# Kernel optimization log

Hardware: AMD Instinct MI355X
Metric: run time of the kernel (lower is better)

## Reference

```python
import jax, jax.numpy as jnp
import numpy as np


def setup_inputs() -> dict:
    key = jax.random.key(0)
    ks = jax.random.split(key, 7)
    B, T, E, H = 256, 512, 256, 256
    s = 1.0 / np.sqrt(E + H)
    return {
        "embedding": jax.random.normal(ks[0], (B, T, E), dtype=jnp.float32),
        "Wz": jax.random.normal(ks[1], (H, E + H), dtype=jnp.float32) * s,
        "bz": jax.random.normal(ks[2], (H,), dtype=jnp.float32) * s,
        "Wr": jax.random.normal(ks[3], (H, E + H), dtype=jnp.float32) * s,
        "br": jax.random.normal(ks[4], (H,), dtype=jnp.float32) * s,
        "Wm": jax.random.normal(ks[5], (H, E + H), dtype=jnp.float32) * s,
        "bm": jax.random.normal(ks[6], (H,), dtype=jnp.float32) * s,
    }


def reference(embedding, Wz, bz, Wr, br, Wm, bm):
    # embedding: [B, T, E] -> time-major [T, B, E] (matches Encoder.forward transpose)
    emb = jnp.transpose(embedding, (1, 0, 2))
    B = emb.shape[1]
    H = Wz.shape[0]
    h0 = jnp.zeros((B, H), dtype=embedding.dtype)

    def step(h, x):  # x: [B, E], h: [B, H]
        xi = jnp.concatenate([x, h], axis=1)            # [B, E+H]
        z = jax.nn.sigmoid(xi @ Wz.T + bz)              # update gate
        r = jax.nn.sigmoid(xi @ Wr.T + br)              # reset gate
        xm = jnp.concatenate([x, r * h], axis=1)
        h_cand = jnp.tanh(xm @ Wm.T + bm)
        h_new = (1.0 - z) * h + z * h_cand
        return h_new, h_new

    _, hs = jax.lax.scan(step, h0, emb)                 # hs: [T, B, H]
    return jnp.transpose(hs, (1, 0, 2))                 # [B, T, H]
```

## Files before the change

kernel.cpp:

```cpp
#include <hip/hip_runtime.h>

typedef _Float16 half8_t __attribute__((ext_vector_type(8)));
typedef _Float16 half2_t __attribute__((ext_vector_type(2)));
typedef float floatx4 __attribute__((ext_vector_type(4)));

#define B_DIM 256
#define T_DIM 512
#define E_DIM 256
#define H_DIM 256
#define MROWS (B_DIM * T_DIM)

__device__ __forceinline__ half2_t mk2(_Float16 x, _Float16 y) {
    half2_t v; v[0] = x; v[1] = y; return v;
}

__device__ __forceinline__ float fdot2f(half2_t a, half2_t b, float c) {
#if __has_builtin(__builtin_amdgcn_fdot2)
    return __builtin_amdgcn_fdot2(a, b, c, false);
#else
    return c + (float)a[0] * (float)b[0] + (float)a[1] * (float)b[1];
#endif
}

__global__ __launch_bounds__(256, 2) void gemm_x(
    const float* __restrict__ emb,
    const float* __restrict__ Wz, const float* __restrict__ bz,
    const float* __restrict__ Wr, const float* __restrict__ br,
    const float* __restrict__ Wm, const float* __restrict__ bm,
    _Float16* __restrict__ Xz, _Float16* __restrict__ Xr,
    float* __restrict__ Xm)
{
    const int n0 = blockIdx.x * 128;
    const int m0 = blockIdx.y * 128;
    const int gate = n0 >> 8;
    const int ng0 = n0 & 255;
    const float* W    = (gate == 0) ? Wz : (gate == 1) ? Wr : Wm;
    const float* bias = (gate == 0) ? bz : (gate == 1) ? br : bm;

    __shared__ __align__(16) _Float16 lA[128 * 40];
    __shared__ __align__(16) _Float16 lB[128 * 40];

    const int t = threadIdx.x;
    const int lane = t & 63;
    const int wave = t >> 6;
    const int wm = (wave >> 1) * 64;
    const int wn = (wave & 1) * 64;
    const int lq = lane >> 4;
    const int lr = lane & 15;

    floatx4 acc[4][4];
    #pragma unroll
    for (int i = 0; i < 4; ++i)
        #pragma unroll
        for (int j = 0; j < 4; ++j)
            acc[i][j] = (floatx4)0.0f;

    const int srow = t >> 1;
    const int scol = (t & 1) * 16;
    const float* aSrc = emb + (size_t)(m0 + srow) * E_DIM + scol;
    const float* bSrc = W + (size_t)(ng0 + srow) * (E_DIM + H_DIM) + scol;

    for (int k0 = 0; k0 < E_DIM; k0 += 32) {
        float ta[16], tb[16];
        #pragma unroll
        for (int u = 0; u < 4; ++u) {
            *(float4*)(ta + 4 * u) = *(const float4*)(aSrc + k0 + 4 * u);
            *(float4*)(tb + 4 * u) = *(const float4*)(bSrc + k0 + 4 * u);
        }
        half8_t a0, a1, b0, b1;
        #pragma unroll
        for (int u = 0; u < 8; ++u) {
            a0[u] = (_Float16)ta[u]; a1[u] = (_Float16)ta[u + 8];
            b0[u] = (_Float16)tb[u]; b1[u] = (_Float16)tb[u + 8];
        }
        __syncthreads();
        *(half8_t*)&lA[srow * 40 + scol]     = a0;
        *(half8_t*)&lA[srow * 40 + scol + 8] = a1;
        *(half8_t*)&lB[srow * 40 + scol]     = b0;
        *(half8_t*)&lB[srow * 40 + scol + 8] = b1;
        __syncthreads();

        half8_t af[4], bf[4];
        #pragma unroll
        for (int i = 0; i < 4; ++i)
            af[i] = *(const half8_t*)&lA[(wm + i * 16 + lr) * 40 + lq * 8];
        #pragma unroll
        for (int j = 0; j < 4; ++j)
            bf[j] = *(const half8_t*)&lB[(wn + j * 16 + lr) * 40 + lq * 8];
        #pragma unroll
        for (int i = 0; i < 4; ++i)
            #pragma unroll
            for (int j = 0; j < 4; ++j)
                acc[i][j] = __builtin_amdgcn_mfma_f32_16x16x32_f16(
                    af[i], bf[j], acc[i][j], 0, 0, 0);
    }

    if (gate < 2) {
        _Float16* dst = (gate == 0) ? Xz : Xr;
        #pragma unroll
        for (int j = 0; j < 4; ++j) {
            const int ng = ng0 + wn + j * 16 + lr;
            const float bv = bias[ng];
            #pragma unroll
            for (int i = 0; i < 4; ++i) {
                const int mrow = m0 + wm + i * 16 + lq * 4;
                #pragma unroll
                for (int r = 0; r < 4; ++r)
                    dst[(size_t)(mrow + r) * H_DIM + ng] =
                        (_Float16)(acc[i][j][r] + bv);
            }
        }
    } else {
        #pragma unroll
        for (int j = 0; j < 4; ++j) {
            const int ng = ng0 + wn + j * 16 + lr;
            const float bv = bias[ng];
            #pragma unroll
            for (int i = 0; i < 4; ++i) {
                const int mrow = m0 + wm + i * 16 + lq * 4;
                #pragma unroll
                for (int r = 0; r < 4; ++r)
                    Xm[(size_t)(mrow + r) * H_DIM + ng] = acc[i][j][r] + bv;
            }
        }
    }
}

__global__ __launch_bounds__(512, 2) void gru_rec(
    const float* __restrict__ Wz,
    const float* __restrict__ Wr,
    const float* __restrict__ Wm,
    const _Float16* __restrict__ Xz,
    const _Float16* __restrict__ Xr,
    float* __restrict__ out)
{
    const int b = blockIdx.x;
    const int t = threadIdx.x;
    const int jA = t & 255;
    const int jB = t >> 1;
    const int hB = t & 1;

    __shared__ __align__(16) _Float16 hh[256];
    __shared__ float hf[256];
    __shared__ __align__(16) _Float16 rh[256];
    __shared__ float zl[256];

    half2_t w1[128];
    {
        const float* wrow = ((t < 256) ? Wz : Wr) + (size_t)jA * 512 + 256;
        #pragma unroll
        for (int k = 0; k < 64; ++k) {
            float4 f = ((const float4*)wrow)[k];
            w1[2 * k]     = mk2((_Float16)f.x, (_Float16)f.y);
            w1[2 * k + 1] = mk2((_Float16)f.z, (_Float16)f.w);
        }
    }
    half2_t w2[64];
    {
        const float* wrow = Wm + (size_t)jB * 512 + 256 + hB * 128;
        #pragma unroll
        for (int k = 0; k < 32; ++k) {
            float4 f = ((const float4*)wrow)[k];
            w2[2 * k]     = mk2((_Float16)f.x, (_Float16)f.y);
            w2[2 * k + 1] = mk2((_Float16)f.z, (_Float16)f.w);
        }
    }

    if (t < 256) { hh[t] = (_Float16)0.0f; hf[t] = 0.0f; }
    __syncthreads();

    const size_t rowbase = (size_t)b * T_DIM * H_DIM;
    float xa_n = (t < 256) ? (float)Xz[rowbase + jA] : (float)Xr[rowbase + jA];
    float xm_n = (hB == 0) ? out[rowbase + jB] : 0.0f;

    for (int ts = 0; ts < T_DIM; ++ts) {
        const float xa = xa_n;
        const float xm = xm_n;
        if (ts + 1 < T_DIM) {
            const size_t nb = rowbase + (size_t)(ts + 1) * H_DIM;
            xa_n = (t < 256) ? (float)Xz[nb + jA] : (float)Xr[nb + jA];
            xm_n = (hB == 0) ? out[nb + jB] : 0.0f;
        }

        float a0 = xa, a1 = 0.f, a2 = 0.f, a3 = 0.f;
        const half8_t* hp8 = (const half8_t*)hh;
        #pragma unroll
        for (int k = 0; k < 32; ++k) {
            half8_t hv = hp8[k];
            a0 = fdot2f(w1[4 * k],     mk2(hv[0], hv[1]), a0);
            a1 = fdot2f(w1[4 * k + 1], mk2(hv[2], hv[3]), a1);
            a2 = fdot2f(w1[4 * k + 2], mk2(hv[4], hv[5]), a2);
            a3 = fdot2f(w1[4 * k + 3], mk2(hv[6], hv[7]), a3);
        }
        const float a = (a0 + a1) + (a2 + a3);
        const float g = 1.0f / (1.0f + __expf(-a));
        if (t < 256) zl[jA] = g;
        else         rh[jA] = (_Float16)(g * hf[jA]);
        __syncthreads();

        float c0 = 0.f, c1 = 0.f;
        const half8_t* rp8 = (const half8_t*)(rh + hB * 128);
        #pragma unroll
        for (int k = 0; k < 16; ++k) {
            half8_t rv = rp8[k];
            c0 = fdot2f(w2[4 * k],     mk2(rv[0], rv[1]), c0);
            c1 = fdot2f(w2[4 * k + 1], mk2(rv[2], rv[3]), c1);
            c0 = fdot2f(w2[4 * k + 2], mk2(rv[4], rv[5]), c0);
            c1 = fdot2f(w2[4 * k + 3], mk2(rv[6], rv[7]), c1);
        }
        float c = c0 + c1;
        c += __shfl_xor(c, 1);
        if (hB == 0) {
            const float am = c + xm;
            const float hcand = 2.0f / (1.0f + __expf(-2.0f * am)) - 1.0f;
            const float z = zl[jB];
            const float hn = (1.0f - z) * hf[jB] + z * hcand;
            out[rowbase + (size_t)ts * H_DIM + jB] = hn;
            hf[jB] = hn;
            hh[jB] = (_Float16)hn;
        }
        __syncthreads();
    }
}

extern "C" void kernel_launch(void* const* d_in, const int* in_sizes, int n_in,
                              void* d_out, int out_size, void* d_ws, size_t ws_size,
                              hipStream_t stream) {
    (void)in_sizes; (void)n_in; (void)out_size; (void)ws_size;
    const float* emb = (const float*)d_in[0];
    const float* Wz  = (const float*)d_in[1];
    const float* bz  = (const float*)d_in[2];
    const float* Wr  = (const float*)d_in[3];
    const float* br  = (const float*)d_in[4];
    const float* Wm  = (const float*)d_in[5];
    const float* bm  = (const float*)d_in[6];
    float* out = (float*)d_out;

    _Float16* Xz = (_Float16*)d_ws;
    _Float16* Xr = Xz + (size_t)MROWS * H_DIM;

    dim3 g1(6, MROWS / 128);
    gemm_x<<<g1, 256, 0, stream>>>(emb, Wz, bz, Wr, br, Wm, bm, Xz, Xr, out);
    gru_rec<<<B_DIM, 512, 0, stream>>>(Wz, Wr, Wm, Xz, Xr, out);
}
```

Baseline: 1.190 ms.

## Use MFMA for recurrent matvecs in GRU step instead of fdot2 loops

Result: faster. 1.019 ms (-14.3%).

```diff
diff --git a/kernel.cpp b/kernel.cpp
--- a/kernel.cpp
+++ b/kernel.cpp
@@ -12,14 +12,6 @@
 
 __device__ __forceinline__ half2_t mk2(_Float16 x, _Float16 y) {
     half2_t v; v[0] = x; v[1] = y; return v;
-}
-
-__device__ __forceinline__ float fdot2f(half2_t a, half2_t b, float c) {
-#if __has_builtin(__builtin_amdgcn_fdot2)
-    return __builtin_amdgcn_fdot2(a, b, c, false);
-#else
-    return c + (float)a[0] * (float)b[0] + (float)a[1] * (float)b[1];
-#endif
 }
 
 __global__ __launch_bounds__(256, 2) void gemm_x(
@@ -126,6 +118,12 @@
     }
 }
 
+__device__ __forceinline__ float pick4(floatx4 v, int r) {
+    float x01 = (r & 1) ? v[1] : v[0];
+    float x23 = (r & 1) ? v[3] : v[2];
+    return (r & 2) ? x23 : x01;
+}
+
 __global__ __launch_bounds__(512, 2) void gru_rec(
     const float* __restrict__ Wz,
     const float* __restrict__ Wr,
@@ -136,88 +134,121 @@
 {
     const int b = blockIdx.x;
     const int t = threadIdx.x;
-    const int jA = t & 255;
-    const int jB = t >> 1;
-    const int hB = t & 1;
+    const int w    = t >> 6;
+    const int lane = t & 63;
+    const int lr   = lane & 15;
+    const int lq   = lane >> 4;
 
     __shared__ __align__(16) _Float16 hh[256];
-    __shared__ float hf[256];
+    __shared__ __align__(16) float    hf[256];
     __shared__ __align__(16) _Float16 rh[256];
-    __shared__ float zl[256];
-
-    half2_t w1[128];
+    __shared__ __align__(16) float    zl[256];
+
+    half8_t af[4][8];
     {
-        const float* wrow = ((t < 256) ? Wz : Wr) + (size_t)jA * 512 + 256;
-        #pragma unroll
-        for (int k = 0; k < 64; ++k) {
-            float4 f = ((const float4*)wrow)[k];
-            w1[2 * k]     = mk2((_Float16)f.x, (_Float16)f.y);
-            w1[2 * k + 1] = mk2((_Float16)f.z, (_Float16)f.w);
-        }
-    }
-    half2_t w2[64];
+        const float* Wg = (w < 4) ? Wz : Wr;
+        #pragma unroll
+        for (int i = 0; i < 4; ++i) {
+            const float* rp = Wg +
+                (size_t)(((w & 3) * 4 + i) * 16 + lr) * (E_DIM + H_DIM) +
+                E_DIM + lq * 8;
+            #pragma unroll
+            for (int kt = 0; kt < 8; ++kt) {
+                float4 f0 = *(const float4*)(rp + kt * 32);
+                float4 f1 = *(const float4*)(rp + kt * 32 + 4);
+                half8_t hv;
+                hv[0] = (_Float16)f0.x; hv[1] = (_Float16)f0.y;
+                hv[2] = (_Float16)f0.z; hv[3] = (_Float16)f0.w;
+                hv[4] = (_Float16)f1.x; hv[5] = (_Float16)f1.y;
+                hv[6] = (_Float16)f1.z; hv[7] = (_Float16)f1.w;
+                af[i][kt] = hv;
+            }
+        }
+    }
+    half8_t am[2][8];
     {
-        const float* wrow = Wm + (size_t)jB * 512 + 256 + hB * 128;
-        #pragma unroll
-        for (int k = 0; k < 32; ++k) {
-            float4 f = ((const float4*)wrow)[k];
-            w2[2 * k]     = mk2((_Float16)f.x, (_Float16)f.y);
-            w2[2 * k + 1] = mk2((_Float16)f.z, (_Float16)f.w);
+        #pragma unroll
+        for (int i = 0; i < 2; ++i) {
+            const float* rp = Wm +
+                (size_t)((w * 2 + i) * 16 + lr) * (E_DIM + H_DIM) +
+                E_DIM + lq * 8;
+            #pragma unroll
+            for (int kt = 0; kt < 8; ++kt) {
+                float4 f0 = *(const float4*)(rp + kt * 32);
+                float4 f1 = *(const float4*)(rp + kt * 32 + 4);
+                half8_t hv;
+                hv[0] = (_Float16)f0.x; hv[1] = (_Float16)f0.y;
+                hv[2] = (_Float16)f0.z; hv[3] = (_Float16)f0.w;
+                hv[4] = (_Float16)f1.x; hv[5] = (_Float16)f1.y;
+                hv[6] = (_Float16)f1.z; hv[7] = (_Float16)f1.w;
+                am[i][kt] = hv;
+            }
         }
     }
 
     if (t < 256) { hh[t] = (_Float16)0.0f; hf[t] = 0.0f; }
     __syncthreads();
 
+    const int rowA = (w & 3) * 64 + (lr >> 2) * 16 + lq * 4 + (lr & 3);
+    const int row2 = w * 32 + ((lr >> 2) & 1) * 16 + lq * 4 + (lr & 3);
+
     const size_t rowbase = (size_t)b * T_DIM * H_DIM;
-    float xa_n = (t < 256) ? (float)Xz[rowbase + jA] : (float)Xr[rowbase + jA];
-    float xm_n = (hB == 0) ? out[rowbase + jB] : 0.0f;
+    const _Float16* Xg = (w < 4) ? Xz : Xr;
+
+    _Float16 xg_p = Xg[rowbase + rowA];
+    float    xm_p = (lr < 8) ? out[rowbase + row2] : 0.0f;
 
     for (int ts = 0; ts < T_DIM; ++ts) {
-        const float xa = xa_n;
-        const float xm = xm_n;
-        if (ts + 1 < T_DIM) {
-            const size_t nb = rowbase + (size_t)(ts + 1) * H_DIM;
-            xa_n = (t < 256) ? (float)Xz[nb + jA] : (float)Xr[nb + jA];
-            xm_n = (hB == 0) ? out[nb + jB] : 0.0f;
-        }
-
-        float a0 = xa, a1 = 0.f, a2 = 0.f, a3 = 0.f;
-        const half8_t* hp8 = (const half8_t*)hh;
-        #pragma unroll
-        for (int k = 0; k < 32; ++k) {
-            half8_t hv = hp8[k];
-            a0 = fdot2f(w1[4 * k],     mk2(hv[0], hv[1]), a0);
-            a1 = fdot2f(w1[4 * k + 1], mk2(hv[2], hv[3]), a1);
-            a2 = fdot2f(w1[4 * k + 2], mk2(hv[4], hv[5]), a2);
-            a3 = fdot2f(w1[4 * k + 3], mk2(hv[6], hv[7]), a3);
-        }
-        const float a = (a0 + a1) + (a2 + a3);
-        const float g = 1.0f / (1.0f + __expf(-a));
-        if (t < 256) zl[jA] = g;
-        else         rh[jA] = (_Float16)(g * hf[jA]);
-        __syncthreads();
-
-        float c0 = 0.f, c1 = 0.f;
-        const half8_t* rp8 = (const half8_t*)(rh + hB * 128);
-        #pragma unroll
-        for (int k = 0; k < 16; ++k) {
-            half8_t rv = rp8[k];
-            c0 = fdot2f(w2[4 * k],     mk2(rv[0], rv[1]), c0);
-            c1 = fdot2f(w2[4 * k + 1], mk2(rv[2], rv[3]), c1);
-            c0 = fdot2f(w2[4 * k + 2], mk2(rv[4], rv[5]), c0);
-            c1 = fdot2f(w2[4 * k + 3], mk2(rv[6], rv[7]), c1);
-        }
-        float c = c0 + c1;
-        c += __shfl_xor(c, 1);
-        if (hB == 0) {
-            const float am = c + xm;
-            const float hcand = 2.0f / (1.0f + __expf(-2.0f * am)) - 1.0f;
-            const float z = zl[jB];
-            const float hn = (1.0f - z) * hf[jB] + z * hcand;
-            out[rowbase + (size_t)ts * H_DIM + jB] = hn;
-            hf[jB] = hn;
-            hh[jB] = (_Float16)hn;
+        floatx4 acc[4];
+        acc[0] = (floatx4)0.0f; acc[1] = (floatx4)0.0f;
+        acc[2] = (floatx4)0.0f; acc[3] = (floatx4)0.0f;
+        #pragma unroll
+        for (int kt = 0; kt < 8; ++kt) {
+            half8_t bf = *(const half8_t*)&hh[kt * 32 + lq * 8];
+            #pragma unroll
+            for (int i = 0; i < 4; ++i)
+                acc[i] = __builtin_amdgcn_mfma_f32_16x16x32_f16(
+                    af[i][kt], bf, acc[i], 0, 0, 0);
+        }
+        {
+            const int r = lr & 3;
+            float s0 = pick4(acc[0], r), s1 = pick4(acc[1], r);
+            float s2 = pick4(acc[2], r), s3 = pick4(acc[3], r);
+            float v = (lr & 8) ? ((lr & 4) ? s3 : s2)
+                               : ((lr & 4) ? s1 : s0);
+            const float a = v + (float)xg_p;
+            const float g = 1.0f / (1.0f + __expf(-a));
+            if (w < 4) zl[rowA] = g;
+            else       rh[rowA] = (_Float16)(g * hf[rowA]);
+        }
+        if (ts + 1 < T_DIM)
+            xg_p = Xg[rowbase + (size_t)(ts + 1) * H_DIM + rowA];
+        __syncthreads();
+
+        floatx4 acc2[2];
+        acc2[0] = (floatx4)0.0f; acc2[1] = (floatx4)0.0f;
+        #pragma unroll
+        for (int kt = 0; kt < 8; ++kt) {
+            half8_t bfm = *(const half8_t*)&rh[kt * 32 + lq * 8];
+            #pragma unroll
+            for (int i = 0; i < 2; ++i)
+                acc2[i] = __builtin_amdgcn_mfma_f32_16x16x32_f16(
+                    am[i][kt], bfm, acc2[i], 0, 0, 0);
+        }
+        if (lr < 8) {
+            const int r = lr & 3;
+            float u0 = pick4(acc2[0], r), u1 = pick4(acc2[1], r);
+            float v2 = (lr & 4) ? u1 : u0;
+            const float amv = v2 + xm_p;
+            const float hc  = 2.0f / (1.0f + __expf(-2.0f * amv)) - 1.0f;
+            const float z   = zl[row2];
+            const float hp  = hf[row2];
+            const float hn  = hp + z * (hc - hp);
+            out[rowbase + (size_t)ts * H_DIM + row2] = hn;
+            hf[row2] = hn;
+            hh[row2] = (_Float16)hn;
+            if (ts + 1 < T_DIM)
+                xm_p = out[rowbase + (size_t)(ts + 1) * H_DIM + row2];
         }
         __syncthreads();
     }
```
